# Kernel optimization log

Hardware: AMD Instinct MI355X
Metric: run time of the kernel (lower is better)

Reference implementation:

```python
import jax, jax.numpy as jnp
import numpy as np

N_NODES = 4096
N_EDGES = 131072
IN_DIM = 40
HID = 128
OUT = 128
GAT_H = 2
GAT_C = 64
D_MODEL = 128
N_HEAD = 4
FF_DIM = 2048
N_LAYERS = 2
EPS = 1e-5
NEG_SLOPE = 0.2


def _layer_norm(x, g, b):
    mu = x.mean(-1, keepdims=True)
    var = ((x - mu) ** 2).mean(-1, keepdims=True)
    return (x - mu) / jnp.sqrt(var + EPS) * g + b


def _gat_conv(h, src, dst, W, a_src, a_dst, bias):
    # PyG GATConv, concat=True, eval mode (no dropout). Self loops already in (src, dst).
    N = h.shape[0]
    xw = (h @ W.T).reshape(N, GAT_H, GAT_C)          # [N, H, C]
    al_src = (xw * a_src).sum(-1)                     # [N, H]
    al_dst = (xw * a_dst).sum(-1)                     # [N, H]
    e = jax.nn.leaky_relu(al_src[src] + al_dst[dst], NEG_SLOPE)  # [E, H]
    # segment softmax over incoming edges of each dst node
    m = jax.ops.segment_max(e, dst, num_segments=N)
    ex = jnp.exp(e - m[dst])
    s = jax.ops.segment_sum(ex, dst, num_segments=N)
    alpha = ex / (s[dst] + 1e-16)                     # [E, H]
    out = jax.ops.segment_sum(xw[src] * alpha[..., None], dst, num_segments=N)
    return out.reshape(N, GAT_H * GAT_C) + bias


def _encoder_layer(x, p):
    # post-norm nn.TransformerEncoderLayer, relu FFN, eval mode
    (in_w, in_b, out_w, out_b, ln1_g, ln1_b,
     ff_w1, ff_b1, ff_w2, ff_b2, ln2_g, ln2_b) = p
    S, E = x.shape
    Dh = E // N_HEAD
    qkv = x @ in_w.T + in_b                           # [S, 3E]
    q, k, v = [t.reshape(S, N_HEAD, Dh) for t in jnp.split(qkv, 3, axis=-1)]
    scores = jnp.einsum('shd,thd->hst', q, k) / jnp.asarray(np.sqrt(Dh), x.dtype)
    attn = jax.nn.softmax(scores, axis=-1)            # [H, S, S]
    o = jnp.einsum('hst,thd->shd', attn, v).reshape(S, E) @ out_w.T + out_b
    x = _layer_norm(x + o, ln1_g, ln1_b)
    ff = jax.nn.relu(x @ ff_w1.T + ff_b1) @ ff_w2.T + ff_b2
    return _layer_norm(x + ff, ln2_g, ln2_b)


def _forward(floats, edge_index):
    (x, enc_w1, enc_b1, enc_w2, enc_b2,
     gat_w, gat_asrc, gat_adst, gat_b,
     l0_in_w, l0_in_b, l0_out_w, l0_out_b, l0_ln1_g, l0_ln1_b,
     l0_ff_w1, l0_ff_b1, l0_ff_w2, l0_ff_b2, l0_ln2_g, l0_ln2_b,
     l1_in_w, l1_in_b, l1_out_w, l1_out_b, l1_ln1_g, l1_ln1_b,
     l1_ff_w1, l1_ff_b1, l1_ff_w2, l1_ff_b2, l1_ln2_g, l1_ln2_b) = floats
    N = x.shape[0]
    # encoder MLP
    h = jax.nn.relu(x @ enc_w1.T + enc_b1) @ enc_w2.T + enc_b2
    # add one self loop per node (GATConv add_self_loops semantics)
    loop = jnp.arange(N, dtype=edge_index.dtype)
    src = jnp.concatenate([edge_index[0], loop])
    dst = jnp.concatenate([edge_index[1], loop])
    h = _gat_conv(h, src, dst, gat_w, gat_asrc, gat_adst, gat_b)
    layers = [
        (l0_in_w, l0_in_b, l0_out_w, l0_out_b, l0_ln1_g, l0_ln1_b,
         l0_ff_w1, l0_ff_b1, l0_ff_w2, l0_ff_b2, l0_ln2_g, l0_ln2_b),
        (l1_in_w, l1_in_b, l1_out_w, l1_out_b, l1_ln1_g, l1_ln1_b,
         l1_ff_w1, l1_ff_b1, l1_ff_w2, l1_ff_b2, l1_ln2_g, l1_ln2_b),
    ]
    for p in layers:
        h = _encoder_layer(h, p)
    return h


def setup_inputs() -> dict:
    key = jax.random.key(0)
    ks = jax.random.split(key, 40)
    s = 0.05
    inp = {}
    inp['x'] = jax.random.normal(ks[0], (N_NODES, IN_DIM), dtype=jnp.float32)
    # edges with src != dst (self loops added inside reference)
    src = jax.random.randint(ks[1], (N_EDGES,), 0, N_NODES)
    off = jax.random.randint(ks[2], (N_EDGES,), 1, N_NODES)
    dst = (src + off) % N_NODES
    inp['edge_index'] = jnp.stack([src, dst]).astype(jnp.int64)
    inp['enc_w1'] = jax.random.normal(ks[3], (HID, IN_DIM)) * s
    inp['enc_b1'] = jnp.zeros((HID,), jnp.float32)
    inp['enc_w2'] = jax.random.normal(ks[4], (OUT, HID)) * s
    inp['enc_b2'] = jnp.zeros((OUT,), jnp.float32)
    inp['gat_w'] = jax.random.normal(ks[5], (GAT_H * GAT_C, OUT)) * s
    inp['gat_asrc'] = jax.random.normal(ks[6], (GAT_H, GAT_C)) * s
    inp['gat_adst'] = jax.random.normal(ks[7], (GAT_H, GAT_C)) * s
    inp['gat_b'] = jnp.zeros((GAT_H * GAT_C,), jnp.float32)
    for i in range(N_LAYERS):
        k = jax.random.split(ks[8 + i], 8)
        inp[f'l{i}_in_w'] = jax.random.normal(k[0], (3 * D_MODEL, D_MODEL)) * s
        inp[f'l{i}_in_b'] = jnp.zeros((3 * D_MODEL,), jnp.float32)
        inp[f'l{i}_out_w'] = jax.random.normal(k[1], (D_MODEL, D_MODEL)) * s
        inp[f'l{i}_out_b'] = jnp.zeros((D_MODEL,), jnp.float32)
        inp[f'l{i}_ln1_g'] = jnp.ones((D_MODEL,), jnp.float32)
        inp[f'l{i}_ln1_b'] = jnp.zeros((D_MODEL,), jnp.float32)
        inp[f'l{i}_ff_w1'] = jax.random.normal(k[2], (FF_DIM, D_MODEL)) * s
        inp[f'l{i}_ff_b1'] = jnp.zeros((FF_DIM,), jnp.float32)
        inp[f'l{i}_ff_w2'] = jax.random.normal(k[3], (D_MODEL, FF_DIM)) * s
        inp[f'l{i}_ff_b2'] = jnp.zeros((D_MODEL,), jnp.float32)
        inp[f'l{i}_ln2_g'] = jnp.ones((D_MODEL,), jnp.float32)
        inp[f'l{i}_ln2_b'] = jnp.zeros((D_MODEL,), jnp.float32)
    return inp


def reference(x, edge_index, enc_w1, enc_b1, enc_w2, enc_b2,
              gat_w, gat_asrc, gat_adst, gat_b,
              l0_in_w, l0_in_b, l0_out_w, l0_out_b, l0_ln1_g, l0_ln1_b,
              l0_ff_w1, l0_ff_b1, l0_ff_w2, l0_ff_b2, l0_ln2_g, l0_ln2_b,
              l1_in_w, l1_in_b, l1_out_w, l1_out_b, l1_ln1_g, l1_ln1_b,
              l1_ff_w1, l1_ff_b1, l1_ff_w2, l1_ff_b2, l1_ln2_g, l1_ln2_b):
    floats = (x, enc_w1, enc_b1, enc_w2, enc_b2,
              gat_w, gat_asrc, gat_adst, gat_b,
              l0_in_w, l0_in_b, l0_out_w, l0_out_b, l0_ln1_g, l0_ln1_b,
              l0_ff_w1, l0_ff_b1, l0_ff_w2, l0_ff_b2, l0_ln2_g, l0_ln2_b,
              l1_in_w, l1_in_b, l1_out_w, l1_out_b, l1_ln1_g, l1_ln1_b,
              l1_ff_w1, l1_ff_b1, l1_ff_w2, l1_ff_b2, l1_ln2_g, l1_ln2_b)
    return _forward(floats, edge_index)
```

## Files before the change

### kernel.cpp

```cpp
#include <hip/hip_runtime.h>
#include <hip/hip_bf16.h>

typedef __hip_bfloat16 bf16;

#define N_NODES 4096
#define IN_DIM  40
#define DM      128
#define FF_DIM  2048
#define GAT_H   2
#define GAT_C   64
#define NHEAD   4
#define DH      32
#define LN_EPS  1e-5f
#define KSPLIT  4

typedef short s8v __attribute__((ext_vector_type(8)));
typedef float f4v __attribute__((ext_vector_type(4)));

#define WO_ENC1 0
#define WO_ENC2 8192
#define WO_GAT  24576
#define WO_L(L) (40960 + (L) * 589824)
#define WO_IN(L)  (WO_L(L))
#define WO_OUT(L) (WO_L(L) + 49152)
#define WO_FF1(L) (WO_L(L) + 65536)
#define WO_FF2(L) (WO_L(L) + 327680)
#define WBUF_ELEMS 1220608

__device__ __forceinline__ float anyload(const void* p, size_t i, int isbf) {
    if (isbf) return __bfloat162float(((const bf16*)p)[i]);
    return ((const float*)p)[i];
}
__device__ __forceinline__ int geti(const int* ei, int i, int is64) {
    return is64 ? ei[2 * (size_t)i] : ei[i];
}
__device__ __forceinline__ ushort tob(float v) {
    bf16 b = __float2bfloat16(v);
    return *(ushort*)&b;
}

__global__ void probe_kernel(const void* ones_vec, const int* ei, int* flags,
                             int* __restrict__ deg) {
    int i = blockIdx.x * 256 + threadIdx.x;
    if (i < N_NODES) deg[i] = 0;
    if (i == 0) {
        unsigned u = ((const unsigned*)ones_vec)[0];
        flags[0] = (u == 0x3F803F80u) ? 1 : 0;
        const unsigned* e = (const unsigned*)ei;
        flags[1] = (e[1] == 0u && e[3] == 0u && e[5] == 0u && e[7] == 0u) ? 1 : 0;
    }
}

__global__ __launch_bounds__(256) void wconv_kernel(const void* enc_w1, const void* enc_w2,
                                                    const void* gat_w,
                                                    const void* in_w0, const void* out_w0,
                                                    const void* ff_w10, const void* ff_w20,
                                                    const void* in_w1, const void* out_w1,
                                                    const void* ff_w11, const void* ff_w21,
                                                    ushort* __restrict__ wbuf,
                                                    const int* __restrict__ flags) {
    const int isbf = flags[0];
    int base = (blockIdx.x * 256 + threadIdx.x) * 4;
#pragma unroll
    for (int j = 0; j < 4; ++j) {
        int i = base + j;
        if (i < WO_ENC2) {
            int r = i >> 6, c = i & 63;
            float v = (c < IN_DIM) ? anyload(enc_w1, (size_t)r * IN_DIM + c, isbf) : 0.f;
            wbuf[i] = tob(v);
            continue;
        }
        const void* s;
        int si;
        if      (i < WO_GAT)     { s = enc_w2; si = i - WO_ENC2; }
        else if (i < WO_L(0))    { s = gat_w;  si = i - WO_GAT; }
        else if (i < WO_OUT(0))  { s = in_w0;  si = i - WO_IN(0); }
        else if (i < WO_FF1(0))  { s = out_w0; si = i - WO_OUT(0); }
        else if (i < WO_FF2(0))  { s = ff_w10; si = i - WO_FF1(0); }
        else if (i < WO_L(1))    { s = ff_w20; si = i - WO_FF2(0); }
        else if (i < WO_OUT(1))  { s = in_w1;  si = i - WO_IN(1); }
        else if (i < WO_FF1(1))  { s = out_w1; si = i - WO_OUT(1); }
        else if (i < WO_FF2(1))  { s = ff_w11; si = i - WO_FF1(1); }
        else                     { s = ff_w21; si = i - WO_FF2(1); }
        wbuf[i] = isbf ? ((const ushort*)s)[si] : tob(((const float*)s)[si]);
    }
}

#define K128STR 136

__global__ __launch_bounds__(256) void encgat_kernel(const void* __restrict__ X,
                                                     const void* __restrict__ b1v,
                                                     const void* __restrict__ b2v,
                                                     const ushort* __restrict__ wbuf,
                                                     const void* __restrict__ asrc,
                                                     const void* __restrict__ adst,
                                                     float* __restrict__ xwout,
                                                     float* __restrict__ als,
                                                     float* __restrict__ ald,
                                                     const int* __restrict__ flags) {
    const int isbf = flags[0];
    const int t = threadIdx.x;
    const int w = t >> 6, lane = t & 63;
    const int col = lane & 15, quad = lane >> 4;
    const int row0 = blockIdx.x * 16;
    __shared__ __align__(16) ushort As[16 * K128STR];
    __shared__ __align__(16) ushort Ws[128 * K128STR];
    __shared__ float Cs[16][132];

    {
        int r = t >> 4, c0 = (t & 15) * 4;
#pragma unroll
        for (int j = 0; j < 4; ++j) {
            int c = c0 + j;
            float v = (c < IN_DIM) ? anyload(X, (size_t)(row0 + r) * IN_DIM + c, isbf) : 0.f;
            As[r * K128STR + c] = tob(v);
        }
    }
#pragma unroll
    for (int i = 0; i < 4; ++i) {
        int idx = t + i * 256;
        int r = idx >> 3, c = (idx & 7) * 8;
        *(uint4*)&Ws[r * 72 + c] = *(const uint4*)&wbuf[WO_ENC1 + r * 64 + c];
    }
    __syncthreads();
    f4v zero = {0.f, 0.f, 0.f, 0.f};
    f4v acc1[2] = {zero, zero};
    {
        s8v a0 = *(const s8v*)&As[col * K128STR + quad * 8];
        s8v a1 = *(const s8v*)&As[col * K128STR + 32 + quad * 8];
#pragma unroll
        for (int nc = 0; nc < 2; ++nc) {
            s8v b0 = *(const s8v*)&Ws[(w * 32 + nc * 16 + col) * 72 + quad * 8];
            s8v b1 = *(const s8v*)&Ws[(w * 32 + nc * 16 + col) * 72 + 32 + quad * 8];
            acc1[nc] = __builtin_amdgcn_mfma_f32_16x16x32_bf16(a0, b0, acc1[nc], 0, 0, 0);
            acc1[nc] = __builtin_amdgcn_mfma_f32_16x16x32_bf16(a1, b1, acc1[nc], 0, 0, 0);
        }
    }
    __syncthreads();
#pragma unroll
    for (int nc = 0; nc < 2; ++nc) {
        int cc = w * 32 + nc * 16 + col;
        float bv = anyload(b1v, cc, isbf);
#pragma unroll
        for (int r = 0; r < 4; ++r)
            As[(quad * 4 + r) * K128STR + cc] = tob(fmaxf(acc1[nc][r] + bv, 0.f));
    }
#pragma unroll
    for (int i = 0; i < 8; ++i) {
        int idx = t + i * 256;
        int r = idx >> 4, c = (idx & 15) * 8;
        *(uint4*)&Ws[r * K128STR + c] = *(const uint4*)&wbuf[WO_ENC2 + r * DM + c];
    }
    __syncthreads();
    f4v acc2[2] = {zero, zero};
#pragma unroll
    for (int j = 0; j < 4; ++j) {
        s8v a = *(const s8v*)&As[col * K128STR + j * 32 + quad * 8];
#pragma unroll
        for (int nc = 0; nc < 2; ++nc) {
            s8v b = *(const s8v*)&Ws[(w * 32 + nc * 16 + col) * K128STR + j * 32 + quad * 8];
            acc2[nc] = __builtin_amdgcn_mfma_f32_16x16x32_bf16(a, b, acc2[nc], 0, 0, 0);
        }
    }
    __syncthreads();
#pragma unroll
    for (int nc = 0; nc < 2; ++nc) {
        int cc = w * 32 + nc * 16 + col;
        float bv = anyload(b2v, cc, isbf);
#pragma unroll
        for (int r = 0; r < 4; ++r)
            As[(quad * 4 + r) * K128STR + cc] = tob(acc2[nc][r] + bv);
    }
#pragma unroll
    for (int i = 0; i < 8; ++i) {
        int idx = t + i * 256;
        int r = idx >> 4, c = (idx & 15) * 8;
        *(uint4*)&Ws[r * K128STR + c] = *(const uint4*)&wbuf[WO_GAT + r * DM + c];
    }
    __syncthreads();
    f4v acc3[2] = {zero, zero};
#pragma unroll
    for (int j = 0; j < 4; ++j) {
        s8v a = *(const s8v*)&As[col * K128STR + j * 32 + quad * 8];
#pragma unroll
        for (int nc = 0; nc < 2; ++nc) {
            s8v b = *(const s8v*)&Ws[(w * 32 + nc * 16 + col) * K128STR + j * 32 + quad * 8];
            acc3[nc] = __builtin_amdgcn_mfma_f32_16x16x32_bf16(a, b, acc3[nc], 0, 0, 0);
        }
    }
#pragma unroll
    for (int nc = 0; nc < 2; ++nc) {
        int cc = w * 32 + nc * 16 + col;
#pragma unroll
        for (int r = 0; r < 4; ++r) {
            int row = quad * 4 + r;
            float v = acc3[nc][r];
            xwout[(size_t)(row0 + row) * DM + cc] = v;
            Cs[row][cc] = v;
        }
    }
    __syncthreads();
#pragma unroll
    for (int rr = 0; rr < 4; ++rr) {
        int row = w * 4 + rr;
        float x0 = Cs[row][lane], x1 = Cs[row][64 + lane];
        float s0 = x0 * anyload(asrc, lane, isbf);
        float d0 = x0 * anyload(adst, lane, isbf);
        float s1 = x1 * anyload(asrc, 64 + lane, isbf);
        float d1 = x1 * anyload(adst, 64 + lane, isbf);
#pragma unroll
        for (int o = 32; o >= 1; o >>= 1) {
            s0 += __shfl_xor(s0, o); d0 += __shfl_xor(d0, o);
            s1 += __shfl_xor(s1, o); d1 += __shfl_xor(d1, o);
        }
        if (lane == 0) {
            int n = row0 + row;
            als[n * 2 + 0] = s0; ald[n * 2 + 0] = d0;
            als[n * 2 + 1] = s1; ald[n * 2 + 1] = d1;
        }
    }
}

__global__ __launch_bounds__(256) void gemm32_kernel(const ushort* __restrict__ A,
                                                     const ushort* __restrict__ Wb,
                                                     const void* __restrict__ bias,
                                                     ushort* __restrict__ Cb,
                                                     ushort* __restrict__ vtb,
                                                     int N,
                                                     const int* __restrict__ flags,
                                                     int relu) {
    const int isbf = flags[0];
    const int t = threadIdx.x;
    const int w = t >> 6, lane = t & 63;
    const int col = lane & 15, quad = lane >> 4;
    const int wr = (w & 1) * 16, wc = (w >> 1) * 32;
    const int row0 = blockIdx.y * 32, col0 = blockIdx.x * 64;
    __shared__ __align__(16) ushort As[32 * K128STR];
    __shared__ __align__(16) ushort Ws[64 * K128STR];
#pragma unroll
    for (int i = 0; i < 2; ++i) {
        int idx = t + i * 256;
        int r = idx >> 4, c = (idx & 15) * 8;
        *(uint4*)&As[r * K128STR + c] = *(const uint4*)&A[(size_t)(row0 + r) * DM + c];
    }
#pragma unroll
    for (int i = 0; i < 4; ++i) {
        int idx = t + i * 256;
        int r = idx >> 4, c = (idx & 15) * 8;
        *(uint4*)&Ws[r * K128STR + c] = *(const uint4*)&Wb[(size_t)(col0 + r) * DM + c];
    }
    __syncthreads();
    f4v zero = {0.f, 0.f, 0.f, 0.f};
    f4v acc[2] = {zero, zero};
#pragma unroll
    for (int j = 0; j < 4; ++j) {
        s8v a = *(const s8v*)&As[(wr + col) * K128STR + j * 32 + quad * 8];
#pragma unroll
        for (int nc = 0; nc < 2; ++nc) {
            s8v b = *(const s8v*)&Ws[(wc + nc * 16 + col) * K128STR + j * 32 + quad * 8];
            acc[nc] = __builtin_amdgcn_mfma_f32_16x16x32_bf16(a, b, acc[nc], 0, 0, 0);
        }
    }
#pragma unroll
    for (int nc = 0; nc < 2; ++nc) {
        int cc = col0 + wc + nc * 16 + col;
        float bv = bias ? anyload(bias, cc, isbf) : 0.f;
#pragma unroll
        for (int r = 0; r < 4; ++r) {
            int rr = row0 + wr + quad * 4 + r;
            float v = acc[nc][r] + bv;
            if (relu) v = fmaxf(v, 0.f);
            Cb[(size_t)rr * N + cc] = tob(v);
            if (vtb && cc >= 256) vtb[(size_t)(cc - 256) * N_NODES + rr] = tob(v);
        }
    }
}

__global__ __launch_bounds__(256) void oproj_ln_kernel(const float* __restrict__ pO,
                                                       const float* __restrict__ pL,
                                                       const ushort* __restrict__ Wb,
                                                       const void* __restrict__ bias,
                                                       float* __restrict__ h,
                                                       ushort* __restrict__ hb,
                                                       const void* __restrict__ g,
                                                       const void* __restrict__ b,
                                                       const int* __restrict__ flags) {
    const int isbf = flags[0];
    const int t = threadIdx.x;
    const int w = t >> 6, lane = t & 63;
    const int col = lane & 15, quad = lane >> 4;
    const int row0 = blockIdx.x * 16;
    __shared__ __align__(16) ushort As[16 * K128STR];
    __shared__ __align__(16) ushort Ws[128 * K128STR];
    __shared__ float Cs[16][132];

    {
        int ar = t >> 4, ac = (t & 15) * 8;
        int rr = row0 + ar;
        int hh = ac >> 5, d0 = ac & 31;
        size_t qi0 = ((size_t)rr) * NHEAD + hh;
        float lsum = 0.f;
        float osum[8] = {};
#pragma unroll
        for (int kz = 0; kz < KSPLIT; ++kz) {
            size_t qi = qi0 + (size_t)kz * N_NODES * NHEAD;
            lsum += pL[qi];
            const float* po = &pO[qi * 32 + d0];
#pragma unroll
            for (int j = 0; j < 8; ++j) osum[j] += po[j];
        }
        float inv = 1.f / lsum;
#pragma unroll
        for (int j = 0; j < 8; ++j) As[ar * K128STR + ac + j] = tob(osum[j] * inv);
    }
#pragma unroll
    for (int i = 0; i < 8; ++i) {
        int idx = t + i * 256;
        int r = idx >> 4, c = (idx & 15) * 8;
        *(uint4*)&Ws[r * K128STR + c] = *(const uint4*)&Wb[(size_t)r * DM + c];
    }
    __syncthreads();
    f4v zero = {0.f, 0.f, 0.f, 0.f};
    f4v acc[2] = {zero, zero};
#pragma unroll
    for (int j = 0; j < 4; ++j) {
        s8v a = *(const s8v*)&As[col * K128STR + j * 32 + quad * 8];
#pragma unroll
        for (int nc = 0; nc < 2; ++nc) {
            s8v b = *(const s8v*)&Ws[(w * 32 + nc * 16 + col) * K128STR + j * 32 + quad * 8];
            acc[nc] = __builtin_amdgcn_mfma_f32_16x16x32_bf16(a, b, acc[nc], 0, 0, 0);
        }
    }
#pragma unroll
    for (int nc = 0; nc < 2; ++nc) {
        int cc = w * 32 + nc * 16 + col;
        float bv = bias ? anyload(bias, cc, isbf) : 0.f;
#pragma unroll
        for (int r = 0; r < 4; ++r)
            Cs[quad * 4 + r][cc] = acc[nc][r] + bv;
    }
    __syncthreads();
#pragma unroll
    for (int rr = 0; rr < 4; ++rr) {
        int row = w * 4 + rr;
        size_t base = (size_t)(row0 + row) * DM;
        float v0 = h[base + lane] + Cs[row][lane];
        float v1 = h[base + 64 + lane] + Cs[row][64 + lane];
        float s = v0 + v1;
#pragma unroll
        for (int o = 32; o >= 1; o >>= 1) s += __shfl_xor(s, o);
        float mu = s * (1.f / DM);
        float d0 = v0 - mu, d1 = v1 - mu;
        float q = d0 * d0 + d1 * d1;
#pragma unroll
        for (int o = 32; o >= 1; o >>= 1) q += __shfl_xor(q, o);
        float rstd = rsqrtf(q * (1.f / DM) + LN_EPS);
        float o0 = d0 * rstd * anyload(g, lane, isbf) + anyload(b, lane, isbf);
        float o1 = d1 * rstd * anyload(g, 64 + lane, isbf) + anyload(b, 64 + lane, isbf);
        h[base + lane] = o0;       h[base + 64 + lane] = o1;
        hb[base + lane] = tob(o0); hb[base + 64 + lane] = tob(o1);
    }
}

__global__ __launch_bounds__(512) void ff2ln_kernel(const ushort* __restrict__ A,
                                                    const ushort* __restrict__ Wb,
                                                    const void* __restrict__ fbias,
                                                    float* __restrict__ h,
                                                    ushort* __restrict__ hb,
                                                    const void* __restrict__ g,
                                                    const void* __restrict__ b,
                                                    void* __restrict__ outp,
                                                    const int* __restrict__ flags) {
    const int isbf = flags[0];
    const int t = threadIdx.x;
    const int w = t >> 6, lane = t & 63;
    const int col = lane & 15, quad = lane >> 4;
    const int row0 = blockIdx.x * 16;
    __shared__ __align__(16) ushort As[16 * K128STR];
    __shared__ __align__(16) ushort Ws[128 * K128STR];
    __shared__ float Cs[16][132];
    f4v zero = {0.f, 0.f, 0.f, 0.f};
    f4v acc = zero;
    for (int k0 = 0; k0 < FF_DIM; k0 += 128) {
        __syncthreads();
        if (t < 256) {
            int ar = t >> 4, ac = (t & 15) * 8;
            *(uint4*)&As[ar * K128STR + ac] =
                *(const uint4*)&A[(size_t)(row0 + ar) * FF_DIM + k0 + ac];
        }
#pragma unroll
        for (int i = 0; i < 4; ++i) {
            int idx = t + i * 512;
            int r = idx >> 4, c = (idx & 15) * 8;
            *(uint4*)&Ws[r * K128STR + c] = *(const uint4*)&Wb[(size_t)r * FF_DIM + k0 + c];
        }
        __syncthreads();
#pragma unroll
        for (int j = 0; j < 4; ++j) {
            s8v a = *(const s8v*)&As[col * K128STR + j * 32 + quad * 8];
            s8v bb = *(const s8v*)&Ws[(w * 16 + col) * K128STR + j * 32 + quad * 8];
            acc = __builtin_amdgcn_mfma_f32_16x16x32_bf16(a, bb, acc, 0, 0, 0);
        }
    }
    {
        int cc = w * 16 + col;
        float bv = anyload(fbias, cc, isbf);
#pragma unroll
        for (int r = 0; r < 4; ++r)
            Cs[quad * 4 + r][cc] = acc[r] + bv;
    }
    __syncthreads();
#pragma unroll
    for (int rr = 0; rr < 2; ++rr) {
        int row = w * 2 + rr;
        size_t base = (size_t)(row0 + row) * DM;
        float v0 = h[base + lane] + Cs[row][lane];
        float v1 = h[base + 64 + lane] + Cs[row][64 + lane];
        float s = v0 + v1;
#pragma unroll
        for (int o = 32; o >= 1; o >>= 1) s += __shfl_xor(s, o);
        float mu = s * (1.f / DM);
        float d0 = v0 - mu, d1 = v1 - mu;
        float q = d0 * d0 + d1 * d1;
#pragma unroll
        for (int o = 32; o >= 1; o >>= 1) q += __shfl_xor(q, o);
        float rstd = rsqrtf(q * (1.f / DM) + LN_EPS);
        float o0 = d0 * rstd * anyload(g, lane, isbf) + anyload(b, lane, isbf);
        float o1 = d1 * rstd * anyload(g, 64 + lane, isbf) + anyload(b, 64 + lane, isbf);
        h[base + lane] = o0;       h[base + 64 + lane] = o1;
        hb[base + lane] = tob(o0); hb[base + 64 + lane] = tob(o1);
        if (outp) {
            if (isbf) {
                ((ushort*)outp)[base + lane] = tob(o0);
                ((ushort*)outp)[base + 64 + lane] = tob(o1);
            } else {
                ((float*)outp)[base + lane] = o0;
                ((float*)outp)[base + 64 + lane] = o1;
            }
        }
    }
}

__global__ void deg_hist_kernel(const int* __restrict__ ei, int E0,
                                int* __restrict__ deg, const int* __restrict__ flags) {
    const int is64 = flags[1];
    int e = blockIdx.x * 256 + threadIdx.x;
    int E = E0 + N_NODES;
    if (e >= E) return;
    int d = (e < E0) ? geti(ei, E0 + e, is64) : (e - E0);
    atomicAdd(&deg[d], 1);
}

__global__ __launch_bounds__(256) void scan_kernel(const int* __restrict__ deg,
                                                   int* __restrict__ rowptr,
                                                   int* __restrict__ cursor) {
    __shared__ int part[256];
    const int t = threadIdx.x;
    const int base = t * 16;
    int loc[16];
    int s = 0;
#pragma unroll
    for (int i = 0; i < 16; ++i) { loc[i] = s; s += deg[base + i]; }
    part[t] = s;
    __syncthreads();
    for (int d = 1; d < 256; d <<= 1) {
        int v = (t >= d) ? part[t - d] : 0;
        __syncthreads();
        part[t] += v;
        __syncthreads();
    }
    int prev = (t == 0) ? 0 : part[t - 1];
#pragma unroll
    for (int i = 0; i < 16; ++i) {
        int r = prev + loc[i];
        rowptr[base + i] = r;
        cursor[base + i] = r;
    }
    if (t == 255) rowptr[N_NODES] = part[255];
}

__global__ void scatter_kernel(const int* __restrict__ ei, int E0,
                               int* __restrict__ cursor, int* __restrict__ csr_src,
                               const int* __restrict__ flags) {
    const int is64 = flags[1];
    int e = blockIdx.x * 256 + threadIdx.x;
    int E = E0 + N_NODES;
    if (e >= E) return;
    int s = (e < E0) ? geti(ei, e, is64) : (e - E0);
    int d = (e < E0) ? geti(ei, E0 + e, is64) : (e - E0);
    int pos = atomicAdd(&cursor[d], 1);
    csr_src[pos] = s;
}

__global__ __launch_bounds__(256) void gat_gather_kernel(const int* __restrict__ rowptr,
                                                         const int* __restrict__ csr_src,
                                                         const float* __restrict__ als,
                                                         const float* __restrict__ ald,
                                                         const float* __restrict__ xw,
                                                         const void* __restrict__ gat_b,
                                                         float* __restrict__ hg,
                                                         ushort* __restrict__ hgb,
                                                         const int* __restrict__ flags) {
    const int isbf = flags[0];
    const int idx = blockIdx.x * 4 + (threadIdx.x >> 6);
    const int lane = threadIdx.x & 63;
    const int d = idx >> 1, hh = idx & 1;
    const int beg = rowptr[d], end = rowptr[d + 1];
    const float aldv = ald[d * 2 + hh];

    float mx = -3.0e38f;
    for (int i = beg + lane; i < end; i += 64) {
        int s = csr_src[i];
        float v = als[s * 2 + hh] + aldv;
        v = (v > 0.f) ? v : 0.2f * v;
        mx = fmaxf(mx, v);
    }
#pragma unroll
    for (int o = 32; o >= 1; o >>= 1) mx = fmaxf(mx, __shfl_xor(mx, o));
    float sm = 0.f;
    for (int i = beg + lane; i < end; i += 64) {
        int s = csr_src[i];
        float v = als[s * 2 + hh] + aldv;
        v = (v > 0.f) ? v : 0.2f * v;
        sm += __expf(v - mx);
    }
#pragma unroll
    for (int o = 32; o >= 1; o >>= 1) sm += __shfl_xor(sm, o);
    const float inv = 1.f / (sm + 1e-16f);

    float o_acc = 0.f;
    for (int i = beg; i < end; ++i) {
        int s = csr_src[i];
        float v = als[s * 2 + hh] + aldv;
        v = (v > 0.f) ? v : 0.2f * v;
        float alpha = __expf(v - mx) * inv;
        o_acc += alpha * xw[(size_t)s * DM + hh * GAT_C + lane];
    }
    float outv = o_acc + anyload(gat_b, hh * GAT_C + lane, isbf);
    size_t off = (size_t)d * DM + hh * GAT_C + lane;
    hg[off] = outv;
    hgb[off] = tob(outv);
}

#define KSTR 40
#define VSTR 136
#define PSTR 136
__global__ __launch_bounds__(256) void attn_mfma_kernel(const ushort* __restrict__ qkvb,
                                                        const ushort* __restrict__ vtb,
                                                        float* __restrict__ pO,
                                                        float* __restrict__ pL) {
    const int hh = blockIdx.y;
    const int kz = blockIdx.z;
    const int t = threadIdx.x;
    const int w = t >> 6;
    const int lane = t & 63;
    const int col = lane & 15;
    const int quad = lane >> 4;
    const int qr = blockIdx.x * 64 + w * 16;

    __shared__ __align__(16) ushort Ks[128 * KSTR];
    __shared__ __align__(16) ushort Vt[32 * VSTR];
    __shared__ __align__(16) ushort Pl[4][16 * PSTR];

    s8v aq = *(const s8v*)&qkvb[(size_t)(qr + col) * 384 + hh * 32 + quad * 8];

    f4v zero = {0.f, 0.f, 0.f, 0.f};
    f4v of[2] = {zero, zero};
    float lacc[4] = {0.f, 0.f, 0.f, 0.f};
    const float scale = 0.17677669529663687f;
    const int k_beg = kz * (N_NODES / KSPLIT);
    const int k_end = k_beg + (N_NODES / KSPLIT);

    for (int kt = k_beg; kt < k_end; kt += 128) {
        __syncthreads();
        for (int idx = t; idx < 512; idx += 256) {
            int r = idx >> 2, c = (idx & 3) * 8;
            *(uint4*)&Ks[r * KSTR + c] =
                *(const uint4*)&qkvb[(size_t)(kt + r) * 384 + 128 + hh * 32 + c];
        }
        for (int idx = t; idx < 512; idx += 256) {
            int d = idx >> 4, c = (idx & 15) * 8;
            *(uint4*)&Vt[d * VSTR + c] =
                *(const uint4*)&vtb[(size_t)(hh * 32 + d) * N_NODES + kt + c];
        }
        __syncthreads();

        f4v sf[8];
#pragma unroll
        for (int kb = 0; kb < 8; ++kb) {
            s8v bk = *(const s8v*)&Ks[(kb * 16 + col) * KSTR + quad * 8];
            sf[kb] = __builtin_amdgcn_mfma_f32_16x16x32_bf16(aq, bk, zero, 0, 0, 0);
        }
#pragma unroll
        for (int kb = 0; kb < 8; ++kb) {
#pragma unroll
            for (int r = 0; r < 4; ++r) {
                float p = __expf(sf[kb][r] * scale);
                lacc[r] += p;
                Pl[w][(quad * 4 + r) * PSTR + kb * 16 + col] = tob(p);
            }
        }
#pragma unroll
        for (int kc = 0; kc < 4; ++kc) {
            s8v ap = *(const s8v*)&Pl[w][col * PSTR + kc * 32 + quad * 8];
#pragma unroll
            for (int nc = 0; nc < 2; ++nc) {
                s8v bv = *(const s8v*)&Vt[(nc * 16 + col) * VSTR + kc * 32 + quad * 8];
                of[nc] = __builtin_amdgcn_mfma_f32_16x16x32_bf16(ap, bv, of[nc], 0, 0, 0);
            }
        }
    }
#pragma unroll
    for (int r = 0; r < 4; ++r) {
        float lv = lacc[r];
#pragma unroll
        for (int off = 1; off <= 8; off <<= 1) lv += __shfl_xor(lv, off);
        int row = quad * 4 + r;
        size_t qi = ((size_t)kz * N_NODES + qr + row) * NHEAD + hh;
#pragma unroll
        for (int nc = 0; nc < 2; ++nc)
            pO[qi * 32 + nc * 16 + col] = of[nc][r];
        if (col == 0) pL[qi] = lv;
    }
}

extern "C" void kernel_launch(void* const* d_in, const int* in_sizes, int n_in,
                              void* d_out, int out_size, void* d_ws, size_t ws_size,
                              hipStream_t stream) {
    const void* x        = d_in[0];
    const int*  ei       = (const int*)d_in[1];
    const void* enc_w1   = d_in[2];
    const void* enc_b1   = d_in[3];
    const void* enc_w2   = d_in[4];
    const void* enc_b2   = d_in[5];
    const void* gat_w    = d_in[6];
    const void* gat_asrc = d_in[7];
    const void* gat_adst = d_in[8];
    const void* gat_b    = d_in[9];
    const void *in_w[2], *in_b[2], *out_w[2], *out_b[2], *ln1_g[2], *ln1_b[2];
    const void *ff_w1[2], *ff_b1[2], *ff_w2[2], *ff_b2[2], *ln2_g[2], *ln2_b[2];
    for (int L = 0; L < 2; ++L) {
        int base = 10 + L * 12;
        in_w[L]  = d_in[base + 0];
        in_b[L]  = d_in[base + 1];
        out_w[L] = d_in[base + 2];
        out_b[L] = d_in[base + 3];
        ln1_g[L] = d_in[base + 4];
        ln1_b[L] = d_in[base + 5];
        ff_w1[L] = d_in[base + 6];
        ff_b1[L] = d_in[base + 7];
        ff_w2[L] = d_in[base + 8];
        ff_b2[L] = d_in[base + 9];
        ln2_g[L] = d_in[base + 10];
        ln2_b[L] = d_in[base + 11];
    }
    const int E0 = in_sizes[1] / 2;
    const int E  = E0 + N_NODES;
    const size_t NN = N_NODES;

    int*    flags   = (int*)d_ws;
    float*  h       = (float*)d_ws + 64;
    ushort* hb      = (ushort*)(h + NN * DM);
    ushort* qkvb    = hb + NN * DM;
    ushort* vtb     = qkvb + NN * 384;
    ushort* ff1b    = vtb + NN * DM;
    ushort* wbuf    = ff1b + NN * FF_DIM;
    float*  pO      = (float*)(wbuf + WBUF_ELEMS);
    float*  pL      = pO + (size_t)KSPLIT * NN * NHEAD * 32;
    float*  xw      = pL + (size_t)KSPLIT * NN * NHEAD;
    float*  als     = xw + NN * DM;
    float*  ald     = als + NN * GAT_H;
    int*    deg     = (int*)(ald + NN * GAT_H);
    int*    rowptr  = deg + N_NODES;
    int*    cursor  = rowptr + N_NODES + 1;
    int*    csr_src = cursor + N_NODES;

    dim3 blk(256);

    probe_kernel<<<dim3(16), blk, 0, stream>>>(ln1_g[0], ei, flags, deg);
    wconv_kernel<<<dim3(WBUF_ELEMS / 1024), blk, 0, stream>>>(
        enc_w1, enc_w2, gat_w, in_w[0], out_w[0], ff_w1[0], ff_w2[0],
        in_w[1], out_w[1], ff_w1[1], ff_w2[1], wbuf, flags);
    deg_hist_kernel<<<dim3((E + 255) / 256), blk, 0, stream>>>(ei, E0, deg, flags);
    scan_kernel<<<dim3(1), blk, 0, stream>>>(deg, rowptr, cursor);
    scatter_kernel<<<dim3((E + 255) / 256), blk, 0, stream>>>(ei, E0, cursor, csr_src, flags);

    encgat_kernel<<<dim3(N_NODES / 16), blk, 0, stream>>>(
        x, enc_b1, enc_b2, wbuf, gat_asrc, gat_adst, xw, als, ald, flags);
    gat_gather_kernel<<<dim3(N_NODES * GAT_H / 4), blk, 0, stream>>>(
        rowptr, csr_src, als, ald, xw, gat_b, h, hb, flags);

    for (int L = 0; L < 2; ++L) {
        gemm32_kernel<<<dim3(3 * DM / 64, N_NODES / 32), blk, 0, stream>>>(
            hb, wbuf + WO_IN(L), in_b[L], qkvb, vtb, 3 * DM, flags, 0);
        attn_mfma_kernel<<<dim3(N_NODES / 64, NHEAD, KSPLIT), blk, 0, stream>>>(
            qkvb, vtb, pO, pL);
        oproj_ln_kernel<<<dim3(N_NODES / 16), blk, 0, stream>>>(
            pO, pL, wbuf + WO_OUT(L), out_b[L], h, hb, ln1_g[L], ln1_b[L], flags);
        gemm32_kernel<<<dim3(FF_DIM / 64, N_NODES / 32), blk, 0, stream>>>(
            hb, wbuf + WO_FF1(L), ff_b1[L], ff1b, nullptr, FF_DIM, flags, 1);
        ff2ln_kernel<<<dim3(N_NODES / 16), dim3(512), 0, stream>>>(
            ff1b, wbuf + WO_FF2(L), ff_b2[L], h, hb, ln2_g[L], ln2_b[L],
            (L == 1) ? d_out : nullptr, flags);
    }
}
```

Baseline: 330.4 us.

## Split FF2 GEMM into split-K tiled kernel plus separate residual-layernorm kernel

Replaces the fused FF2+layernorm kernel (16 rows per block, one MFMA tile per wave, reloading the full 128x2048 weight per 16 rows) with a split-K GEMM that uses 64-row tiles and 8 accumulators per wave. Partial sums over 4 K-slices go to a new fp32 workspace and are reduced by a separate bias+residual+layernorm kernel. This cuts redundant weight traffic and raises MFMA reuse, at the cost of an extra launch and partial-sum round-trips. It also merges the probe and weight-conversion setup kernels into one launch.

```diff
diff --git a/kernel.cpp b/kernel.cpp
--- a/kernel.cpp
+++ b/kernel.cpp
@@ -13,6 +13,7 @@
 #define DH      32
 #define LN_EPS  1e-5f
 #define KSPLIT  4
+#define FSPLIT  4
 
 typedef short s8v __attribute__((ext_vector_type(8)));
 typedef float f4v __attribute__((ext_vector_type(4)));
@@ -39,31 +40,28 @@
     return *(ushort*)&b;
 }
 
-__global__ void probe_kernel(const void* ones_vec, const int* ei, int* flags,
-                             int* __restrict__ deg) {
-    int i = blockIdx.x * 256 + threadIdx.x;
-    if (i < N_NODES) deg[i] = 0;
-    if (i == 0) {
-        unsigned u = ((const unsigned*)ones_vec)[0];
-        flags[0] = (u == 0x3F803F80u) ? 1 : 0;
-        const unsigned* e = (const unsigned*)ei;
-        flags[1] = (e[1] == 0u && e[3] == 0u && e[5] == 0u && e[7] == 0u) ? 1 : 0;
-    }
-}
-
-__global__ __launch_bounds__(256) void wconv_kernel(const void* enc_w1, const void* enc_w2,
+__global__ __launch_bounds__(256) void setup_kernel(const void* ones_vec, const int* ei,
+                                                    int* flags, int* __restrict__ deg,
+                                                    const void* enc_w1, const void* enc_w2,
                                                     const void* gat_w,
                                                     const void* in_w0, const void* out_w0,
                                                     const void* ff_w10, const void* ff_w20,
                                                     const void* in_w1, const void* out_w1,
                                                     const void* ff_w11, const void* ff_w21,
-                                                    ushort* __restrict__ wbuf,
-                                                    const int* __restrict__ flags) {
-    const int isbf = flags[0];
-    int base = (blockIdx.x * 256 + threadIdx.x) * 4;
+                                                    ushort* __restrict__ wbuf) {
+    const int isbf = (((const unsigned*)ones_vec)[0] == 0x3F803F80u) ? 1 : 0;
+    int gid = blockIdx.x * 256 + threadIdx.x;
+    if (gid < N_NODES) deg[gid] = 0;
+    if (gid == 0) {
+        flags[0] = isbf;
+        const unsigned* e = (const unsigned*)ei;
+        flags[1] = (e[1] == 0u && e[3] == 0u && e[5] == 0u && e[7] == 0u) ? 1 : 0;
+    }
+    int base = gid * 4;
 #pragma unroll
     for (int j = 0; j < 4; ++j) {
         int i = base + j;
+        if (i >= WBUF_ELEMS) break;
         if (i < WO_ENC2) {
             int r = i >> 6, c = i & 63;
             float v = (c < IN_DIM) ? anyload(enc_w1, (size_t)r * IN_DIM + c, isbf) : 0.f;
@@ -362,81 +360,98 @@
     }
 }
 
-__global__ __launch_bounds__(512) void ff2ln_kernel(const ushort* __restrict__ A,
-                                                    const ushort* __restrict__ Wb,
-                                                    const void* __restrict__ fbias,
-                                                    float* __restrict__ h,
-                                                    ushort* __restrict__ hb,
-                                                    const void* __restrict__ g,
-                                                    const void* __restrict__ b,
-                                                    void* __restrict__ outp,
-                                                    const int* __restrict__ flags) {
-    const int isbf = flags[0];
+__global__ __launch_bounds__(256) void ff2_splitk_kernel(const ushort* __restrict__ A,
+                                                         const ushort* __restrict__ Wb,
+                                                         float* __restrict__ Cpart) {
     const int t = threadIdx.x;
     const int w = t >> 6, lane = t & 63;
     const int col = lane & 15, quad = lane >> 4;
-    const int row0 = blockIdx.x * 16;
-    __shared__ __align__(16) ushort As[16 * K128STR];
+    const int row0 = blockIdx.x * 64;
+    const int ks = blockIdx.y;
+    const int k_beg = ks * (FF_DIM / FSPLIT);
+    __shared__ __align__(16) ushort As[64 * K128STR];
     __shared__ __align__(16) ushort Ws[128 * K128STR];
-    __shared__ float Cs[16][132];
     f4v zero = {0.f, 0.f, 0.f, 0.f};
-    f4v acc = zero;
-    for (int k0 = 0; k0 < FF_DIM; k0 += 128) {
+    f4v acc[8] = {zero, zero, zero, zero, zero, zero, zero, zero};
+    const int wr = w * 16;
+
+    for (int it = 0; it < 4; ++it) {
+        int k0 = k_beg + it * 128;
         __syncthreads();
-        if (t < 256) {
-            int ar = t >> 4, ac = (t & 15) * 8;
-            *(uint4*)&As[ar * K128STR + ac] =
-                *(const uint4*)&A[(size_t)(row0 + ar) * FF_DIM + k0 + ac];
-        }
 #pragma unroll
         for (int i = 0; i < 4; ++i) {
-            int idx = t + i * 512;
+            int idx = t + i * 256;
+            int r = idx >> 4, c = (idx & 15) * 8;
+            *(uint4*)&As[r * K128STR + c] = *(const uint4*)&A[(size_t)(row0 + r) * FF_DIM + k0 + c];
+        }
+#pragma unroll
+        for (int i = 0; i < 8; ++i) {
+            int idx = t + i * 256;
             int r = idx >> 4, c = (idx & 15) * 8;
             *(uint4*)&Ws[r * K128STR + c] = *(const uint4*)&Wb[(size_t)r * FF_DIM + k0 + c];
         }
         __syncthreads();
 #pragma unroll
         for (int j = 0; j < 4; ++j) {
-            s8v a = *(const s8v*)&As[col * K128STR + j * 32 + quad * 8];
-            s8v bb = *(const s8v*)&Ws[(w * 16 + col) * K128STR + j * 32 + quad * 8];
-            acc = __builtin_amdgcn_mfma_f32_16x16x32_bf16(a, bb, acc, 0, 0, 0);
-        }
-    }
-    {
-        int cc = w * 16 + col;
-        float bv = anyload(fbias, cc, isbf);
-#pragma unroll
-        for (int r = 0; r < 4; ++r)
-            Cs[quad * 4 + r][cc] = acc[r] + bv;
-    }
-    __syncthreads();
-#pragma unroll
-    for (int rr = 0; rr < 2; ++rr) {
-        int row = w * 2 + rr;
-        size_t base = (size_t)(row0 + row) * DM;
-        float v0 = h[base + lane] + Cs[row][lane];
-        float v1 = h[base + 64 + lane] + Cs[row][64 + lane];
-        float s = v0 + v1;
-#pragma unroll
-        for (int o = 32; o >= 1; o >>= 1) s += __shfl_xor(s, o);
-        float mu = s * (1.f / DM);
-        float d0 = v0 - mu, d1 = v1 - mu;
-        float q = d0 * d0 + d1 * d1;
-#pragma unroll
-        for (int o = 32; o >= 1; o >>= 1) q += __shfl_xor(q, o);
-        float rstd = rsqrtf(q * (1.f / DM) + LN_EPS);
-        float o0 = d0 * rstd * anyload(g, lane, isbf) + anyload(b, lane, isbf);
-        float o1 = d1 * rstd * anyload(g, 64 + lane, isbf) + anyload(b, 64 + lane, isbf);
-        h[base + lane] = o0;       h[base + 64 + lane] = o1;
-        hb[base + lane] = tob(o0); hb[base + 64 + lane] = tob(o1);
-        if (outp) {
-            if (isbf) {
-                ((ushort*)outp)[base + lane] = tob(o0);
-                ((ushort*)outp)[base + 64 + lane] = tob(o1);
-            } else {
-                ((float*)outp)[base + lane] = o0;
-                ((float*)outp)[base + 64 + lane] = o1;
+            s8v a = *(const s8v*)&As[(wr + col) * K128STR + j * 32 + quad * 8];
+#pragma unroll
+            for (int nc = 0; nc < 8; ++nc) {
+                s8v b = *(const s8v*)&Ws[(nc * 16 + col) * K128STR + j * 32 + quad * 8];
+                acc[nc] = __builtin_amdgcn_mfma_f32_16x16x32_bf16(a, b, acc[nc], 0, 0, 0);
             }
+        }
+    }
+#pragma unroll
+    for (int nc = 0; nc < 8; ++nc) {
+        int cc = nc * 16 + col;
+#pragma unroll
+        for (int r = 0; r < 4; ++r) {
+            int rr = row0 + wr + quad * 4 + r;
+            Cpart[((size_t)ks * N_NODES + rr) * DM + cc] = acc[nc][r];
+        }
+    }
+}
+
+__global__ __launch_bounds__(256) void ln4_kernel(float* __restrict__ h,
+                                                  const float* __restrict__ pC,
+                                                  const void* __restrict__ fbias,
+                                                  ushort* __restrict__ hb,
+                                                  const void* __restrict__ g, const void* __restrict__ b,
+                                                  void* __restrict__ outp,
+                                                  const int* __restrict__ flags) {
+    const int isbf = flags[0];
+    const int row = blockIdx.x * 4 + (threadIdx.x >> 6);
+    const int lane = threadIdx.x & 63;
+    const size_t base = (size_t)row * DM;
+    float y0 = anyload(fbias, lane, isbf), y1 = anyload(fbias, 64 + lane, isbf);
+#pragma unroll
+    for (int kz = 0; kz < FSPLIT; ++kz) {
+        size_t pb = (size_t)kz * N_NODES * DM + base;
+        y0 += pC[pb + lane];
+        y1 += pC[pb + 64 + lane];
+    }
+    float v0 = h[base + lane] + y0;
+    float v1 = h[base + 64 + lane] + y1;
+    float s = v0 + v1;
+#pragma unroll
+    for (int o = 32; o >= 1; o >>= 1) s += __shfl_xor(s, o);
+    float mu = s * (1.f / DM);
+    float d0 = v0 - mu, d1 = v1 - mu;
+    float q = d0 * d0 + d1 * d1;
+#pragma unroll
+    for (int o = 32; o >= 1; o >>= 1) q += __shfl_xor(q, o);
+    float rstd = rsqrtf(q * (1.f / DM) + LN_EPS);
+    float o0 = d0 * rstd * anyload(g, lane, isbf) + anyload(b, lane, isbf);
+    float o1 = d1 * rstd * anyload(g, 64 + lane, isbf) + anyload(b, 64 + lane, isbf);
+    h[base + lane] = o0;       h[base + 64 + lane] = o1;
+    hb[base + lane] = tob(o0); hb[base + 64 + lane] = tob(o1);
+    if (outp) {
+        if (isbf) {
+            ((ushort*)outp)[base + lane] = tob(o0);
+            ((ushort*)outp)[base + 64 + lane] = tob(o1);
+        } else {
+            ((float*)outp)[base + lane] = o0;
+            ((float*)outp)[base + 64 + lane] = o1;
         }
     }
 }
@@ -667,7 +682,8 @@
     ushort* wbuf    = ff1b + NN * FF_DIM;
     float*  pO      = (float*)(wbuf + WBUF_ELEMS);
     float*  pL      = pO + (size_t)KSPLIT * NN * NHEAD * 32;
-    float*  xw      = pL + (size_t)KSPLIT * NN * NHEAD;
+    float*  pC      = pL + (size_t)KSPLIT * NN * NHEAD;
+    float*  xw      = pC + (size_t)FSPLIT * NN * DM;
     float*  als     = xw + NN * DM;
     float*  ald     = als + NN * GAT_H;
     int*    deg     = (int*)(ald + NN * GAT_H);
@@ -677,10 +693,10 @@
 
     dim3 blk(256);
 
-    probe_kernel<<<dim3(16), blk, 0, stream>>>(ln1_g[0], ei, flags, deg);
-    wconv_kernel<<<dim3(WBUF_ELEMS / 1024), blk, 0, stream>>>(
+    setup_kernel<<<dim3((WBUF_ELEMS + 1023) / 1024), blk, 0, stream>>>(
+        ln1_g[0], ei, flags, deg,
         enc_w1, enc_w2, gat_w, in_w[0], out_w[0], ff_w1[0], ff_w2[0],
-        in_w[1], out_w[1], ff_w1[1], ff_w2[1], wbuf, flags);
+        in_w[1], out_w[1], ff_w1[1], ff_w2[1], wbuf);
     deg_hist_kernel<<<dim3((E + 255) / 256), blk, 0, stream>>>(ei, E0, deg, flags);
     scan_kernel<<<dim3(1), blk, 0, stream>>>(deg, rowptr, cursor);
     scatter_kernel<<<dim3((E + 255) / 256), blk, 0, stream>>>(ei, E0, cursor, csr_src, flags);
@@ -699,8 +715,10 @@
             pO, pL, wbuf + WO_OUT(L), out_b[L], h, hb, ln1_g[L], ln1_b[L], flags);
         gemm32_kernel<<<dim3(FF_DIM / 64, N_NODES / 32), blk, 0, stream>>>(
             hb, wbuf + WO_FF1(L), ff_b1[L], ff1b, nullptr, FF_DIM, flags, 1);
-        ff2ln_kernel<<<dim3(N_NODES / 16), dim3(512), 0, stream>>>(
-            ff1b, wbuf + WO_FF2(L), ff_b2[L], h, hb, ln2_g[L], ln2_b[L],
+        ff2_splitk_kernel<<<dim3(N_NODES / 64, FSPLIT), blk, 0, stream>>>(
+            ff1b, wbuf + WO_FF2(L), pC);
+        ln4_kernel<<<dim3(N_NODES / 4), blk, 0, stream>>>(
+            h, pC, ff_b2[L], hb, ln2_g[L], ln2_b[L],
             (L == 1) ? d_out : nullptr, flags);
     }
 }
```

Result: faster. 318.1 us, median of 2 (-3.7%).
